# Kernel optimization log

Hardware: AMD Instinct MI355X
Metric: run time of the kernel (lower is better)

## Reference

```python
import jax, jax.numpy as jnp
import numpy as np

EPS = 1e-09  # present in module but unused in forward math

def setup_inputs() -> dict:
    key = jax.random.key(0)
    k1, k2 = jax.random.split(key)
    n, d = 4096, 512
    outputs = jax.random.normal(k1, (n, d), dtype=jnp.float32)
    labels = jax.random.randint(k2, (n,), 0, 100, dtype=jnp.int64)
    return {"outputs": outputs, "labels": labels, "margin": 1.0}

def reference(outputs, labels, margin):
    # Pairwise squared L2 distances D[i,j] = ||x_i - x_j||^2 via expansion.
    sq = jnp.sum(outputs * outputs, axis=-1)                     # [n]
    D = sq[:, None] + sq[None, :] - 2.0 * (outputs @ outputs.T)  # [n, n]
    D = jnp.maximum(D, 0.0)
    same = (labels[:, None] == labels[None, :])                  # [n, n] bool; includes diagonal
    zn1 = jnp.sum(same)
    zn2 = same.size - zn1
    sum1 = jnp.sum(jnp.where(same, D, 0.0))
    sum2 = jnp.sum(jnp.where(same, 0.0, jnp.maximum(0.0, margin - D)))
    return 0.5 * (sum1 / zn1 + sum2 / zn2)
```

## Files before the change

### kernel.cpp

```cpp
#include <hip/hip_runtime.h>
#include <stdint.h>

#define NROWS 4096
#define DIM   512
#define BK    32
#define TILE  128
#define NBLK  32
#define NPAIR 528
#define KSTEPS (DIM / BK)

typedef float f32x4 __attribute__((ext_vector_type(4)));
typedef short s16x8 __attribute__((ext_vector_type(8)));

#define OFF_XB   0u
#define OFF_SQ   (NROWS * DIM * 2u)
#define OFF_LAB  (OFF_SQ + NROWS * 4u)
#define OFF_ACC  (OFF_LAB + NROWS * 4u)

__device__ __forceinline__ unsigned short f2bf(float f) {
  unsigned u = __float_as_uint(f);
  return (unsigned short)((u + 0x7FFFu + ((u >> 16) & 1u)) >> 16);
}

typedef __attribute__((address_space(1))) unsigned int glb_uint;
typedef __attribute__((address_space(3))) unsigned int lds_uint;

__device__ __forceinline__ void gl2lds16(const void* g, void* l) {
  __builtin_amdgcn_global_load_lds(
      (glb_uint*)(uintptr_t)g,
      (lds_uint*)(unsigned int)(uintptr_t)l,
      16, 0, 0);
}

__global__ __launch_bounds__(256) void prep_kernel(
    const float* __restrict__ X, const long long* __restrict__ lab,
    unsigned short* __restrict__ Xb, float* __restrict__ sq,
    int* __restrict__ labi, float* __restrict__ accum)
{
  int t = threadIdx.x;
  int gid = blockIdx.x * 256 + t;
  if (gid < 4) accum[gid] = 0.0f;
  if (gid < NROWS) labi[gid] = (int)lab[gid];

  int wave = t >> 6, lane = t & 63;
  int row = blockIdx.x * 4 + wave;
  const float4* Xr = (const float4*)(X + (size_t)row * DIM);
  float4 a = Xr[lane * 2];
  float4 b = Xr[lane * 2 + 1];

  uint4 pk;
  pk.x = (unsigned)f2bf(a.x) | ((unsigned)f2bf(a.y) << 16);
  pk.y = (unsigned)f2bf(a.z) | ((unsigned)f2bf(a.w) << 16);
  pk.z = (unsigned)f2bf(b.x) | ((unsigned)f2bf(b.y) << 16);
  pk.w = (unsigned)f2bf(b.z) | ((unsigned)f2bf(b.w) << 16);
  *(uint4*)(Xb + (size_t)row * DIM + lane * 8) = pk;

  float s = a.x*a.x + a.y*a.y + a.z*a.z + a.w*a.w
          + b.x*b.x + b.y*b.y + b.z*b.z + b.w*b.w;
  #pragma unroll
  for (int off = 32; off; off >>= 1) s += __shfl_down(s, off, 64);
  if (lane == 0) sq[row] = s;
}

__global__ __launch_bounds__(256) void pair_kernel(
    const unsigned short* __restrict__ Xb, const float* __restrict__ sq,
    const int* __restrict__ labi, const float* __restrict__ marginp,
    float* __restrict__ accum, float* __restrict__ out)
{
  __shared__ unsigned short As[2][4096];
  __shared__ unsigned short Bs[2][4096];
  __shared__ float sRow[TILE], sCol[TILE];
  __shared__ int   lRow[TILE], lCol[TILE];
  __shared__ float rs1[4], rs2[4];
  __shared__ int   rc[4];

  int t = threadIdx.x;

  int rem = blockIdx.x, bi = 0;
  while (rem >= (NBLK - bi)) { rem -= (NBLK - bi); bi++; }
  int bj = bi + rem;

  int wave = t >> 6, lane = t & 63;
  int quad = lane >> 4, ml = lane & 15;
  int waveRow = (wave >> 1) * 64, waveCol = (wave & 1) * 64;

  float margin = *marginp;
  float sqv; int lbv;
  {
    int u = t & 127;
    int base = (t < TILE ? bi : bj) * TILE + u;
    sqv = sq[base];
    lbv = labi[base];
  }

  const int rr = t & 127;
  const int ch = t >> 7;
  const size_t gA = (size_t)(bi * TILE + rr) * DIM + ch * 8;
  const size_t gB = (size_t)(bj * TILE + rr) * DIM + ch * 8;

  f32x4 acc[4][4] = {};

  #define STAGE(buf, kt)                                                      \
    do {                                                                      \
      size_t ko = (size_t)(kt) * BK;                                          \
      gl2lds16(Xb + gA + ko,      (void*)(&As[(buf)][t * 8]));                \
      gl2lds16(Xb + gA + ko + 16, (void*)(&As[(buf)][2048 + t * 8]));         \
      gl2lds16(Xb + gB + ko,      (void*)(&Bs[(buf)][t * 8]));                \
      gl2lds16(Xb + gB + ko + 16, (void*)(&Bs[(buf)][2048 + t * 8]));         \
    } while (0)

  #define COMPUTE(buf)                                                        \
    do {                                                                      \
      const s16x8* Ap = (const s16x8*)As[(buf)];                              \
      const s16x8* Bp = (const s16x8*)Bs[(buf)];                              \
      s16x8 af[4], bfr[4];                                                    \
      _Pragma("unroll")                                                       \
      for (int r = 0; r < 4; ++r)                                             \
        af[r] = Ap[quad * 128 + waveRow + r * 16 + ml];                       \
      _Pragma("unroll")                                                       \
      for (int c = 0; c < 4; ++c)                                             \
        bfr[c] = Bp[quad * 128 + waveCol + c * 16 + ml];                      \
      _Pragma("unroll")                                                       \
      for (int r = 0; r < 4; ++r)                                             \
        _Pragma("unroll")                                                     \
        for (int c = 0; c < 4; ++c)                                           \
          acc[r][c] = __builtin_amdgcn_mfma_f32_16x16x32_bf16(                \
              af[r], bfr[c], acc[r][c], 0, 0, 0);                             \
    } while (0)

  STAGE(0, 0);
  int cur = 0;
  for (int kt = 0; kt < KSTEPS - 1; ++kt) {
    __syncthreads();
    STAGE(cur ^ 1, kt + 1);
    COMPUTE(cur);
    cur ^= 1;
  }
  __syncthreads();
  COMPUTE(cur);

  if (t < TILE) { sRow[t] = sqv; lRow[t] = lbv; }
  else          { sCol[t - TILE] = sqv; lCol[t - TILE] = lbv; }
  __syncthreads();

  float s1 = 0.f, s2 = 0.f;
  int cnt = 0;
  #pragma unroll
  for (int c = 0; c < 4; ++c) {
    int col = waveCol + c * 16 + ml;
    float sqc = sCol[col];
    int lc = lCol[col];
    #pragma unroll
    for (int r = 0; r < 4; ++r) {
      int rbase = waveRow + r * 16 + quad * 4;
      #pragma unroll
      for (int i = 0; i < 4; ++i) {
        int row = rbase + i;
        float d = sRow[row] + sqc - 2.0f * acc[r][c][i];
        d = fmaxf(d, 0.0f);
        if (lRow[row] == lc) { s1 += d; cnt++; }
        else                 { s2 += fmaxf(margin - d, 0.0f); }
      }
    }
  }

  #pragma unroll
  for (int off = 32; off; off >>= 1) {
    s1  += __shfl_down(s1, off, 64);
    s2  += __shfl_down(s2, off, 64);
    cnt += __shfl_down(cnt, off, 64);
  }
  if (lane == 0) { rs1[wave] = s1; rs2[wave] = s2; rc[wave] = cnt; }
  __syncthreads();
  if (t == 0) {
    float f = (bi == bj) ? 1.f : 2.f;
    float S1 = 0.f, S2 = 0.f;
    int C = 0;
    for (int w = 0; w < 4; ++w) { S1 += rs1[w]; S2 += rs2[w]; C += rc[w]; }
    atomicAdd(&accum[0], S1 * f);
    atomicAdd(&accum[1], S2 * f);
    atomicAdd((unsigned*)accum + 2, (unsigned)C * (unsigned)((bi == bj) ? 1 : 2));
    __threadfence();
    unsigned done = atomicAdd((unsigned*)accum + 3, 1u);
    if (done == NPAIR - 1) {
      __threadfence();
      float S1f = atomicAdd(&accum[0], 0.0f);
      float S2f = atomicAdd(&accum[1], 0.0f);
      unsigned c1 = atomicAdd((unsigned*)accum + 2, 0u);
      double zn1 = (double)c1;
      double zn2 = (double)NROWS * (double)NROWS - zn1;
      out[0] = (float)(0.5 * ((double)S1f / zn1 + (double)S2f / zn2));
    }
  }
  #undef STAGE
  #undef COMPUTE
}

extern "C" void kernel_launch(void* const* d_in, const int* in_sizes, int n_in,
                              void* d_out, int out_size, void* d_ws, size_t ws_size,
                              hipStream_t stream) {
  const float*     X      = (const float*)d_in[0];
  const long long* lab    = (const long long*)d_in[1];
  const float*     margin = (const float*)d_in[2];
  float*           out    = (float*)d_out;

  char* ws = (char*)d_ws;
  unsigned short* Xb   = (unsigned short*)(ws + OFF_XB);
  float*          sq   = (float*)(ws + OFF_SQ);
  int*            labi = (int*)(ws + OFF_LAB);
  float*          accum= (float*)(ws + OFF_ACC);

  prep_kernel<<<NROWS / 4, 256, 0, stream>>>(X, lab, Xb, sq, labi, accum);
  pair_kernel<<<NPAIR, 256, 0, stream>>>(Xb, sq, labi, margin, accum, out);
}
```

Before: 116.4 us.

## Replace direct global-to-LDS loads with register-staged prefetch into padded LDS

The tile staging drops the global_load_lds builtin. Each k-step's global loads now go into registers, are issued before the MFMA compute on the current buffer, and are written to the other LDS buffer afterwards. The LDS layout changes from a k-chunk-major arrangement to row-major with a padded pitch of 40 elements, which aims to keep the MFMA operand reads free of bank conflicts. This costs extra VGPRs for the staged data plus explicit LDS store instructions, and it uses slightly more LDS.

```diff
diff --git a/kernel.cpp b/kernel.cpp
--- a/kernel.cpp
+++ b/kernel.cpp
@@ -8,6 +8,7 @@
 #define NBLK  32
 #define NPAIR 528
 #define KSTEPS (DIM / BK)
+#define PITCH 40
 
 typedef float f32x4 __attribute__((ext_vector_type(4)));
 typedef short s16x8 __attribute__((ext_vector_type(8)));
@@ -20,16 +21,6 @@
 __device__ __forceinline__ unsigned short f2bf(float f) {
   unsigned u = __float_as_uint(f);
   return (unsigned short)((u + 0x7FFFu + ((u >> 16) & 1u)) >> 16);
-}
-
-typedef __attribute__((address_space(1))) unsigned int glb_uint;
-typedef __attribute__((address_space(3))) unsigned int lds_uint;
-
-__device__ __forceinline__ void gl2lds16(const void* g, void* l) {
-  __builtin_amdgcn_global_load_lds(
-      (glb_uint*)(uintptr_t)g,
-      (lds_uint*)(unsigned int)(uintptr_t)l,
-      16, 0, 0);
 }
 
 __global__ __launch_bounds__(256) void prep_kernel(
@@ -67,8 +58,8 @@
     const int* __restrict__ labi, const float* __restrict__ marginp,
     float* __restrict__ accum, float* __restrict__ out)
 {
-  __shared__ unsigned short As[2][4096];
-  __shared__ unsigned short Bs[2][4096];
+  __shared__ unsigned short As[2][TILE * PITCH];
+  __shared__ unsigned short Bs[2][TILE * PITCH];
   __shared__ float sRow[TILE], sCol[TILE];
   __shared__ int   lRow[TILE], lCol[TILE];
   __shared__ float rs1[4], rs2[4];
@@ -93,33 +84,47 @@
     lbv = labi[base];
   }
 
-  const int rr = t & 127;
-  const int ch = t >> 7;
-  const size_t gA = (size_t)(bi * TILE + rr) * DIM + ch * 8;
-  const size_t gB = (size_t)(bj * TILE + rr) * DIM + ch * 8;
-
-  f32x4 acc[4][4] = {};
-
-  #define STAGE(buf, kt)                                                      \
+  const int r0 = t >> 2;
+  const int c0 = (t & 3) * 8;
+  const size_t gA0 = (size_t)(bi * TILE +      r0) * DIM + c0;
+  const size_t gA1 = (size_t)(bi * TILE + 64 + r0) * DIM + c0;
+  const size_t gB0 = (size_t)(bj * TILE +      r0) * DIM + c0;
+  const size_t gB1 = (size_t)(bj * TILE + 64 + r0) * DIM + c0;
+  const int wr0 = r0 * PITCH + c0;
+  const int wr1 = (r0 + 64) * PITCH + c0;
+
+  uint4 rA0, rA1, rB0, rB1;
+
+  #define LOADG(kt)                                                           \
     do {                                                                      \
       size_t ko = (size_t)(kt) * BK;                                          \
-      gl2lds16(Xb + gA + ko,      (void*)(&As[(buf)][t * 8]));                \
-      gl2lds16(Xb + gA + ko + 16, (void*)(&As[(buf)][2048 + t * 8]));         \
-      gl2lds16(Xb + gB + ko,      (void*)(&Bs[(buf)][t * 8]));                \
-      gl2lds16(Xb + gB + ko + 16, (void*)(&Bs[(buf)][2048 + t * 8]));         \
+      rA0 = *(const uint4*)(Xb + gA0 + ko);                                   \
+      rA1 = *(const uint4*)(Xb + gA1 + ko);                                   \
+      rB0 = *(const uint4*)(Xb + gB0 + ko);                                   \
+      rB1 = *(const uint4*)(Xb + gB1 + ko);                                   \
     } while (0)
+
+  #define WRITELDS(buf)                                                       \
+    do {                                                                      \
+      *(uint4*)(&As[(buf)][wr0]) = rA0;                                       \
+      *(uint4*)(&As[(buf)][wr1]) = rA1;                                       \
+      *(uint4*)(&Bs[(buf)][wr0]) = rB0;                                       \
+      *(uint4*)(&Bs[(buf)][wr1]) = rB1;                                       \
+    } while (0)
+
+  f32x4 acc[4][4] = {};
 
   #define COMPUTE(buf)                                                        \
     do {                                                                      \
-      const s16x8* Ap = (const s16x8*)As[(buf)];                              \
-      const s16x8* Bp = (const s16x8*)Bs[(buf)];                              \
+      const unsigned short* Ab = As[(buf)];                                   \
+      const unsigned short* Bb = Bs[(buf)];                                   \
       s16x8 af[4], bfr[4];                                                    \
       _Pragma("unroll")                                                       \
       for (int r = 0; r < 4; ++r)                                             \
-        af[r] = Ap[quad * 128 + waveRow + r * 16 + ml];                       \
+        af[r] = *(const s16x8*)(Ab + (waveRow + r * 16 + ml) * PITCH + quad * 8); \
       _Pragma("unroll")                                                       \
       for (int c = 0; c < 4; ++c)                                             \
-        bfr[c] = Bp[quad * 128 + waveCol + c * 16 + ml];                      \
+        bfr[c] = *(const s16x8*)(Bb + (waveCol + c * 16 + ml) * PITCH + quad * 8); \
       _Pragma("unroll")                                                       \
       for (int r = 0; r < 4; ++r)                                             \
         _Pragma("unroll")                                                     \
@@ -128,16 +133,20 @@
               af[r], bfr[c], acc[r][c], 0, 0, 0);                             \
     } while (0)
 
-  STAGE(0, 0);
+  LOADG(0);
+  WRITELDS(0);
+  __syncthreads();
   int cur = 0;
-  for (int kt = 0; kt < KSTEPS - 1; ++kt) {
-    __syncthreads();
-    STAGE(cur ^ 1, kt + 1);
+  #pragma unroll 2
+  for (int kt = 0; kt < KSTEPS; ++kt) {
+    if (kt + 1 < KSTEPS) LOADG(kt + 1);
     COMPUTE(cur);
-    cur ^= 1;
-  }
-  __syncthreads();
-  COMPUTE(cur);
+    if (kt + 1 < KSTEPS) {
+      WRITELDS(cur ^ 1);
+      __syncthreads();
+      cur ^= 1;
+    }
+  }
 
   if (t < TILE) { sRow[t] = sqv; lRow[t] = lbv; }
   else          { sCol[t - TILE] = sqv; lCol[t - TILE] = lbv; }
@@ -192,7 +201,8 @@
       out[0] = (float)(0.5 * ((double)S1f / zn1 + (double)S2f / zn2));
     }
   }
-  #undef STAGE
+  #undef LOADG
+  #undef WRITELDS
   #undef COMPUTE
 }
 
```

After: 111.8 us. 4.0% less time.
